# Performance work log

Hardware: AMD Instinct MI355X
Metric: run time of the kernel (lower is better)

The kernel has to match this reference:

```python
import jax, jax.numpy as jnp
import numpy as np

FONT_NUM = 190
HID = 256
HEADS = 2
EPS = 1e-5


def _bn(x, g, b, m, v):
    # eval-mode BatchNorm over the last (channel) axis
    return (x - m) * (g * jax.lax.rsqrt(v + EPS)) + b


def _gru(x, Wih, Whh, bih, bhh):
    # x: [B, S, D]; PyTorch gate order r, z, n. Returns all hidden states [B, S, H].
    B, S, _ = x.shape
    H = Whh.shape[1]
    xp = x @ Wih.T + bih  # [B, S, 3H] -- one big GEMM for all timesteps
    def step(h, xt):
        gh = h @ Whh.T + bhh
        xr, xz, xn = jnp.split(xt, 3, axis=-1)
        hr, hz, hn = jnp.split(gh, 3, axis=-1)
        r = jax.nn.sigmoid(xr + hr)
        z = jax.nn.sigmoid(xz + hz)
        n = jnp.tanh(xn + r * hn)
        h_new = (1.0 - z) * n + z * h
        return h_new, h_new
    h0 = jnp.zeros((B, H), x.dtype)
    _, hs = jax.lax.scan(step, h0, jnp.swapaxes(xp, 0, 1))
    return jnp.swapaxes(hs, 0, 1)


def _forward(img_emb, text_embs, len_mask, label_mask, labels,
             img_W, img_b, img_g, img_beta, img_m, img_v,
             g1_Wih, g1_Whh, g1_bih, g1_bhh, tl_W, tl_b,
             t_g, t_beta, t_m, t_v,
             g2_Wih, g2_Whh, g2_bih, g2_bhh, cl_W, cl_b,
             c_g, c_beta, c_m, c_v,
             attn_Win, attn_bin, attn_Wout, attn_bout, pred_W, pred_b):
    # img encoder: Linear -> BN -> (Dropout eval=id) -> ReLU
    img_fea = jax.nn.relu(_bn(img_emb @ img_W.T + img_b, img_g, img_beta, img_m, img_v))  # [B,H]
    # text encoder: GRU -> ReLU -> Linear, then BN+ReLU (torch does this in [B,C,S]; equivalent over channels)
    t = jax.nn.relu(_gru(text_embs, g1_Wih, g1_Whh, g1_bih, g1_bhh))
    t = t @ tl_W.T + tl_b
    text_fea = jax.nn.relu(_bn(t, t_g, t_beta, t_m, t_v))  # [B,S,H]
    len_info = len_mask.sum(axis=1)  # [B]
    # NOTE: sum over ALL timesteps divided by valid length (faithful to source)
    mean = text_fea.sum(axis=1) / len_info[:, None]  # [B,H]
    contrast = text_fea - mean[:, None, :]
    c = jax.nn.relu(_gru(contrast, g2_Wih, g2_Whh, g2_bih, g2_bhh))
    c = c @ cl_W.T + cl_b
    contrast_fea = jax.nn.relu(_bn(c, c_g, c_beta, c_m, c_v))  # [B,S,H]
    B, S, H = text_fea.shape
    hd = H // HEADS
    # batched 3-token self-attention: collapse the per-timestep python loop into one call
    tokens = jnp.stack([
        jnp.broadcast_to(img_fea[:, None, :], (B, S, H)), text_fea, contrast_fea
    ], axis=0).reshape(3, B * S, H)  # [3, N, H]
    Wq, Wk, Wv = jnp.split(attn_Win, 3, axis=0)
    bq, bk, bv = jnp.split(attn_bin, 3, axis=0)
    scale = 1.0 / jnp.sqrt(jnp.asarray(hd, tokens.dtype))
    q = (tokens @ Wq.T + bq).reshape(3, B * S, HEADS, hd) * scale
    k = (tokens @ Wk.T + bk).reshape(3, B * S, HEADS, hd)
    v = (tokens @ Wv.T + bv).reshape(3, B * S, HEADS, hd)
    scores = jnp.einsum('tnhd,snhd->nhts', q, k)  # [N, heads, 3, 3]
    attn = jax.nn.softmax(scores, axis=-1)
    o = jnp.einsum('nhts,snhd->tnhd', attn, v).reshape(3, B * S, H)
    o = o @ attn_Wout.T + attn_bout
    last = o.mean(axis=0).reshape(B, S, H)  # att_fea.mean(0) over the 3 tokens
    logits = last @ pred_W.T + pred_b  # [B,S,FONT_NUM]
    pred = jax.nn.softmax(logits, axis=-1)
    oh = jnp.maximum(label_mask, jax.nn.one_hot(labels, FONT_NUM, dtype=pred.dtype))
    loss = -(oh * jnp.log(pred)).sum(axis=-1)  # [B,S]
    loss = (loss * len_mask).sum(axis=1) / len_info
    return loss.mean()


def setup_inputs() -> dict:
    key = jax.random.key(0)
    ks = jax.random.split(key, 16)
    B, S, D, H = 128, 128, 2048, HID
    img_emb = jax.random.normal(ks[0], (B, D), jnp.float32)
    text_embs = jax.random.normal(ks[1], (B, S, D), jnp.float32)
    lengths = jax.random.randint(ks[2], (B,), S // 2, S + 1)
    len_mask = (jnp.arange(S)[None, :] < lengths[:, None]).astype(jnp.float32)
    labels = jax.random.randint(ks[3], (B, S), 0, FONT_NUM)
    label_mask = jnp.zeros((B, S, FONT_NUM), jnp.float32)
    w = lambda k, sh: jax.random.normal(k, sh, jnp.float32) * 0.02
    params = dict(
        img_W=w(ks[4], (H, D)), img_b=jnp.zeros((H,)),
        img_g=jnp.ones((H,)), img_beta=jnp.zeros((H,)), img_m=jnp.zeros((H,)), img_v=jnp.ones((H,)),
        g1_Wih=w(ks[5], (3 * (H // 2), D)), g1_Whh=w(ks[6], (3 * (H // 2), H // 2)),
        g1_bih=jnp.zeros((3 * (H // 2),)), g1_bhh=jnp.zeros((3 * (H // 2),)),
        tl_W=w(ks[7], (H, H // 2)), tl_b=jnp.zeros((H,)),
        t_g=jnp.ones((H,)), t_beta=jnp.zeros((H,)), t_m=jnp.zeros((H,)), t_v=jnp.ones((H,)),
        g2_Wih=w(ks[8], (3 * H, H)), g2_Whh=w(ks[9], (3 * H, H)),
        g2_bih=jnp.zeros((3 * H,)), g2_bhh=jnp.zeros((3 * H,)),
        cl_W=w(ks[10], (H, H)), cl_b=jnp.zeros((H,)),
        c_g=jnp.ones((H,)), c_beta=jnp.zeros((H,)), c_m=jnp.zeros((H,)), c_v=jnp.ones((H,)),
        attn_Win=w(ks[11], (3 * H, H)), attn_bin=jnp.zeros((3 * H,)),
        attn_Wout=w(ks[12], (H, H)), attn_bout=jnp.zeros((H,)),
        pred_W=w(ks[13], (FONT_NUM, H)), pred_b=jnp.zeros((FONT_NUM,)),
    )
    return dict(img_emb=img_emb, text_embs=text_embs, len_mask=len_mask,
                label_mask=label_mask, labels=labels, **params)


def reference(img_emb, text_embs, len_mask, label_mask, labels,
              img_W, img_b, img_g, img_beta, img_m, img_v,
              g1_Wih, g1_Whh, g1_bih, g1_bhh, tl_W, tl_b,
              t_g, t_beta, t_m, t_v,
              g2_Wih, g2_Whh, g2_bih, g2_bhh, cl_W, cl_b,
              c_g, c_beta, c_m, c_v,
              attn_Win, attn_bin, attn_Wout, attn_bout, pred_W, pred_b):
    return _forward(img_emb, text_embs, len_mask, label_mask, labels,
                    img_W, img_b, img_g, img_beta, img_m, img_v,
                    g1_Wih, g1_Whh, g1_bih, g1_bhh, tl_W, tl_b,
                    t_g, t_beta, t_m, t_v,
                    g2_Wih, g2_Whh, g2_bih, g2_bhh, cl_W, cl_b,
                    c_g, c_beta, c_m, c_v,
                    attn_Win, attn_bin, attn_Wout, attn_bout, pred_W, pred_b)
```

## Files before the change

### kernel.cpp

```cpp
#include <hip/hip_runtime.h>

typedef __attribute__((ext_vector_type(8))) short short8;
typedef __attribute__((ext_vector_type(4))) float f32x4;
typedef _Float16 f16;
typedef __attribute__((ext_vector_type(2))) _Float16 f16x2;
typedef __attribute__((ext_vector_type(8))) _Float16 f16x8;

__device__ inline float bf2f(unsigned short u){
  union{float f; unsigned u32;} x; x.u32 = ((unsigned)u) << 16; return x.f;
}
__device__ inline unsigned short f2bf(float f){
  union{float f; unsigned u;} x; x.f = f;
  unsigned r = (x.u + 0x7FFFu + ((x.u >> 16) & 1u)) >> 16;
  return (unsigned short)r;
}

#if defined(__has_builtin)
#  if __has_builtin(__builtin_amdgcn_fdot2)
#    define HAS_FDOT2 1
#  endif
#endif
__device__ inline float dot2f(f16x2 a, f16x2 b, float c){
#ifdef HAS_FDOT2
  return __builtin_amdgcn_fdot2(a, b, c, false);
#else
  return c + (float)a.x * (float)b.x + (float)a.y * (float)b.y;
#endif
}
__device__ inline f16x2 asf16x2(int v){ return __builtin_bit_cast(f16x2, v); }
__device__ inline int pack2(float lo, float hi){
  f16x2 p = f16x2{(f16)lo, (f16)hi};
  return __builtin_bit_cast(int, p);
}

__device__ inline float sigmoidf_(float x){ return 1.f / (1.f + __expf(-x)); }
__device__ inline float tanh_fast(float x){ float e = __expf(2.f * x); return 1.f - 2.f / (e + 1.f); }

__device__ inline float dpp_xor1(float x){
  return __int_as_float(__builtin_amdgcn_update_dpp(0, __float_as_int(x), 0xB1, 0xF, 0xF, true));
}
__device__ inline float dpp_xor2(float x){
  return __int_as_float(__builtin_amdgcn_update_dpp(0, __float_as_int(x), 0x4E, 0xF, 0xF, true));
}

__device__ inline void load8bf(const unsigned short* p, float* o){
  uint4 q = *(const uint4*)p;
  o[0]=bf2f((unsigned short)(q.x & 0xffffu)); o[1]=bf2f((unsigned short)(q.x >> 16));
  o[2]=bf2f((unsigned short)(q.y & 0xffffu)); o[3]=bf2f((unsigned short)(q.y >> 16));
  o[4]=bf2f((unsigned short)(q.z & 0xffffu)); o[5]=bf2f((unsigned short)(q.z >> 16));
  o[6]=bf2f((unsigned short)(q.w & 0xffffu)); o[7]=bf2f((unsigned short)(q.w >> 16));
}

#define GLL16(g, l) __builtin_amdgcn_global_load_lds(                      \
    (const __attribute__((address_space(1))) void*)(g),                    \
    (__attribute__((address_space(3))) void*)(l), 16, 0, 0)

__global__ __launch_bounds__(256) void conv_all_k(
    const float* __restrict__ s0, const float* __restrict__ s1,
    const float* __restrict__ s2, const float* __restrict__ s3,
    const float* __restrict__ s4, const float* __restrict__ s5,
    const float* __restrict__ s6, const float* __restrict__ s7,
    unsigned short* __restrict__ d0, unsigned short* __restrict__ d1,
    unsigned short* __restrict__ d2, f16* __restrict__ d3,
    unsigned short* __restrict__ d4, unsigned short* __restrict__ d5,
    unsigned short* __restrict__ d6, unsigned short* __restrict__ d7)
{
  int i = blockIdx.x * 256 + threadIdx.x;
  if (i >= 516096) return;
  const float* src; int local; int mode = 0; unsigned short* dst = nullptr; f16* dstf = nullptr;
  if (i < 196608)      { src = s0; local = i;           dst = d0; }
  else if (i < 204800) { src = s1; local = i - 196608;  dst = d1; }
  else if (i < 253952) { src = s2; local = i - 204800;  dst = d2; }
  else if (i < 303104) { src = s3; local = i - 253952;  dstf = d3; mode = 1; }
  else if (i < 319488) { src = s4; local = i - 303104;  dst = d4; }
  else if (i < 368640) { src = s5; local = i - 319488;  dst = d5; }
  else if (i < 385024) { src = s6; local = i - 368640;  dst = d6; }
  else                 { src = s7; local = i - 385024;  dst = d7; }
  float4 v = ((const float4*)src)[local];
  if (mode == 0) {
    union { unsigned short s[4]; uint2 q; } u;
    u.s[0]=f2bf(v.x); u.s[1]=f2bf(v.y); u.s[2]=f2bf(v.z); u.s[3]=f2bf(v.w);
    ((uint2*)dst)[local] = u.q;
  } else {
    union { f16 s[4]; uint2 q; } u;
    u.s[0]=(f16)v.x; u.s[1]=(f16)v.y; u.s[2]=(f16)v.z; u.s[3]=(f16)v.w;
    ((uint2*)dstf)[local] = u.q;
  }
}

__global__ __launch_bounds__(256) void pred_pad_k(const float* __restrict__ W,
                                                  const float* __restrict__ b,
                                                  unsigned short* __restrict__ Wd,
                                                  float* __restrict__ bd){
  int i = blockIdx.x * 256 + threadIdx.x;
  int j = i >> 8;
  Wd[i] = (j < 190) ? f2bf(W[i]) : (unsigned short)0;
  if (i < 192) bd[i] = (i < 190) ? b[i] : 0.f;
}

template<int OUT_T, bool BN, int A_MODE>
__global__ __launch_bounds__(256) void gemm128_k(
    const void* __restrict__ Ap, const unsigned short* __restrict__ Bw,
    const float* __restrict__ bias,
    const float* __restrict__ gam, const float* __restrict__ bet,
    const float* __restrict__ mu,  const float* __restrict__ var,
    void* __restrict__ Cp, int M, int N, int K)
{
  __shared__ __align__(16) unsigned short As[4096];
  __shared__ __align__(16) unsigned short Bs[4096];
  const int tid  = threadIdx.x;
  const int lane = tid & 63, wid = tid >> 6;
  const int wm = wid & 1, wn = wid >> 1;
  const int bm = blockIdx.y << 7, bn = blockIdx.x << 7;
  const int rA = tid >> 2, seg = tid & 3;

  f32x4 acc[4][4];
  #pragma unroll
  for (int i = 0; i < 4; i++)
    #pragma unroll
    for (int j = 0; j < 4; j++)
      acc[i][j] = f32x4{0.f, 0.f, 0.f, 0.f};

  const unsigned short* Abf = (const unsigned short*)Ap;
  const float* Af = (const float*)Ap;
  char* asb = (char*)As;
  char* bsb = (char*)Bs;
  char* asw = asb + wid * 1024;
  char* bsw = bsb + wid * 1024;

  for (int k0 = 0; k0 < K; k0 += 32) {
    if (A_MODE == 1) {
      #pragma unroll
      for (int beta = 0; beta < 2; beta++) {
        const float* src = Af + (size_t)(bm + rA + beta * 64) * K + k0 + seg * 8;
        float4 v0 = *(const float4*)src;
        float4 v1 = *(const float4*)(src + 4);
        union { unsigned short s[8]; uint4 q; } u;
        u.s[0]=f2bf(v0.x); u.s[1]=f2bf(v0.y); u.s[2]=f2bf(v0.z); u.s[3]=f2bf(v0.w);
        u.s[4]=f2bf(v1.x); u.s[5]=f2bf(v1.y); u.s[6]=f2bf(v1.z); u.s[7]=f2bf(v1.w);
        *(uint4*)(asb + beta * 4096 + tid * 16) = u.q;
      }
    } else if (A_MODE == 2) {
      const float* mrow = mu + (size_t)(bm >> 7) * 256 + k0 + seg * 8;
      float4 m0 = *(const float4*)mrow;
      float4 m1 = *(const float4*)(mrow + 4);
      #pragma unroll
      for (int beta = 0; beta < 2; beta++) {
        const unsigned short* src = Abf + (size_t)(bm + rA + beta * 64) * K + k0 + seg * 8;
        float av[8];
        load8bf(src, av);
        union { unsigned short s[8]; uint4 q; } u;
        u.s[0]=f2bf(av[0]-m0.x); u.s[1]=f2bf(av[1]-m0.y); u.s[2]=f2bf(av[2]-m0.z); u.s[3]=f2bf(av[3]-m0.w);
        u.s[4]=f2bf(av[4]-m1.x); u.s[5]=f2bf(av[5]-m1.y); u.s[6]=f2bf(av[6]-m1.z); u.s[7]=f2bf(av[7]-m1.w);
        *(uint4*)(asb + beta * 4096 + tid * 16) = u.q;
      }
    } else {
      GLL16(Abf + (size_t)(bm + rA)      * K + k0 + seg * 8, asw);
      GLL16(Abf + (size_t)(bm + rA + 64) * K + k0 + seg * 8, asw + 4096);
    }
    GLL16(Bw + (size_t)(bn + rA)      * K + k0 + seg * 8, bsw);
    GLL16(Bw + (size_t)(bn + rA + 64) * K + k0 + seg * 8, bsw + 4096);
    __syncthreads();

    short8 a[4], b[4];
    #pragma unroll
    for (int f = 0; f < 4; f++) {
      int ra = wm * 64 + f * 16 + (lane & 15);
      a[f] = *(const short8*)(asb + ra * 64 + (lane >> 4) * 16);
      int rb = wn * 64 + f * 16 + (lane & 15);
      b[f] = *(const short8*)(bsb + rb * 64 + (lane >> 4) * 16);
    }
    #pragma unroll
    for (int fm = 0; fm < 4; fm++)
      #pragma unroll
      for (int fn = 0; fn < 4; fn++)
        acc[fm][fn] = __builtin_amdgcn_mfma_f32_16x16x32_bf16(a[fm], b[fn], acc[fm][fn], 0, 0, 0);
    __syncthreads();
  }

  #pragma unroll
  for (int fn = 0; fn < 4; fn++) {
    int col = bn + wn * 64 + fn * 16 + (lane & 15);
    float bs = bias[col];
    float sc = 1.f, sh = 0.f;
    if (BN) { float s = gam[col] * rsqrtf(var[col] + 1e-5f); sc = s; sh = bet[col] - mu[col] * s; }
    #pragma unroll
    for (int fm = 0; fm < 4; fm++) {
      int row = bm + wm * 64 + fm * 16 + ((lane >> 4) << 2);
      #pragma unroll
      for (int j = 0; j < 4; j++) {
        float v = acc[fm][fn][j] + bs;
        if (BN) { v = v * sc + sh; v = fmaxf(v, 0.f); }
        size_t idx = (size_t)(row + j) * N + col;
        if (OUT_T == 1) ((f16*)Cp)[idx] = (f16)v;
        else            ((unsigned short*)Cp)[idx] = f2bf(v);
      }
    }
  }
}

template<int OUT_T, bool BN, bool AF32>
__global__ __launch_bounds__(256) void gemm_k(
    const void* __restrict__ Ap, const unsigned short* __restrict__ Bw,
    const float* __restrict__ bias,
    const float* __restrict__ gam, const float* __restrict__ bet,
    const float* __restrict__ mu,  const float* __restrict__ var,
    void* __restrict__ Cp, int M, int N, int K)
{
  __shared__ unsigned short As[64][40];
  __shared__ unsigned short Bs[64][40];
  const int tid  = threadIdx.x;
  const int lane = tid & 63, wid = tid >> 6;
  const int wm = wid & 1, wn = wid >> 1;
  const int bm = blockIdx.y << 6, bn = blockIdx.x << 6;
  const int srow = tid >> 2, sseg = tid & 3;

  f32x4 acc[2][2];
  #pragma unroll
  for (int i = 0; i < 2; i++)
    #pragma unroll
    for (int j = 0; j < 2; j++)
      acc[i][j] = f32x4{0.f, 0.f, 0.f, 0.f};

  const unsigned short* Abf = (const unsigned short*)Ap;
  const float* Af = (const float*)Ap;

  for (int k0 = 0; k0 < K; k0 += 32) {
    if (AF32) {
      const float* src = Af + (size_t)(bm + srow) * K + k0 + sseg * 8;
      float4 v0 = *(const float4*)(src);
      float4 v1 = *(const float4*)(src + 4);
      union { unsigned short s[8]; uint4 q; } u;
      u.s[0]=f2bf(v0.x); u.s[1]=f2bf(v0.y); u.s[2]=f2bf(v0.z); u.s[3]=f2bf(v0.w);
      u.s[4]=f2bf(v1.x); u.s[5]=f2bf(v1.y); u.s[6]=f2bf(v1.z); u.s[7]=f2bf(v1.w);
      *(uint4*)&As[srow][sseg * 8] = u.q;
    } else {
      *(uint4*)&As[srow][sseg * 8] =
          *(const uint4*)(Abf + (size_t)(bm + srow) * K + k0 + sseg * 8);
    }
    *(uint4*)&Bs[srow][sseg * 8] =
        *(const uint4*)(Bw + (size_t)(bn + srow) * K + k0 + sseg * 8);
    __syncthreads();

    short8 a0 = *(const short8*)&As[wm * 32 +      (lane & 15)][(lane >> 4) * 8];
    short8 a1 = *(const short8*)&As[wm * 32 + 16 + (lane & 15)][(lane >> 4) * 8];
    short8 b0 = *(const short8*)&Bs[wn * 32 +      (lane & 15)][(lane >> 4) * 8];
    short8 b1 = *(const short8*)&Bs[wn * 32 + 16 + (lane & 15)][(lane >> 4) * 8];
    acc[0][0] = __builtin_amdgcn_mfma_f32_16x16x32_bf16(a0, b0, acc[0][0], 0, 0, 0);
    acc[0][1] = __builtin_amdgcn_mfma_f32_16x16x32_bf16(a0, b1, acc[0][1], 0, 0, 0);
    acc[1][0] = __builtin_amdgcn_mfma_f32_16x16x32_bf16(a1, b0, acc[1][0], 0, 0, 0);
    acc[1][1] = __builtin_amdgcn_mfma_f32_16x16x32_bf16(a1, b1, acc[1][1], 0, 0, 0);
    __syncthreads();
  }

  #pragma unroll
  for (int fn = 0; fn < 2; fn++) {
    int col = bn + wn * 32 + fn * 16 + (lane & 15);
    float bs = bias[col];
    float sc = 1.f, sh = 0.f;
    if (BN) { float s = gam[col] * rsqrtf(var[col] + 1e-5f); sc = s; sh = bet[col] - mu[col] * s; }
    #pragma unroll
    for (int fm = 0; fm < 2; fm++) {
      int row = bm + wm * 32 + fm * 16 + ((lane >> 4) << 2);
      #pragma unroll
      for (int j = 0; j < 4; j++) {
        float v = acc[fm][fn][j] + bs;
        if (BN) { v = v * sc + sh; v = fmaxf(v, 0.f); }
        size_t idx = (size_t)(row + j) * N + col;
        if (OUT_T == 0)      ((float*)Cp)[idx] = v;
        else if (OUT_T == 1) ((f16*)Cp)[idx]   = (f16)v;
        else                 ((unsigned short*)Cp)[idx] = f2bf(v);
      }
    }
  }
}

__global__ __launch_bounds__(512, 2) void gru2_scan_k(
    const f16* __restrict__ Wf,
    const float* __restrict__ bhh,
    const f16* __restrict__ xp, unsigned short* __restrict__ hs_relu)
{
  const int b = blockIdx.x;
  const int tid = threadIdx.x;
  const int jj = tid >> 1, kh = tid & 1;
  __shared__ __align__(16) f16 hbuf[2][256];
  __shared__ __align__(16) char wnl[16 * 512 * 16];

  {
    const f16* src = Wf + (size_t)(512 + jj) * 256 + kh * 128;
    #pragma unroll
    for (int c = 0; c < 16; c++)
      *(uint4*)(wnl + c * 8192 + tid * 16) = *(const uint4*)(src + c * 8);
  }

  int wri[64], wzi[64];
  #pragma unroll
  for (int i = 0; i < 16; i++) {
    const int kb = kh * 128 + i * 8;
    uint4 q;
    q = *(const uint4*)&Wf[(size_t)(jj      ) * 256 + kb];
    wri[4*i+0] = (int)q.x; wri[4*i+1] = (int)q.y; wri[4*i+2] = (int)q.z; wri[4*i+3] = (int)q.w;
    q = *(const uint4*)&Wf[(size_t)(jj + 256) * 256 + kb];
    wzi[4*i+0] = (int)q.x; wzi[4*i+1] = (int)q.y; wzi[4*i+2] = (int)q.z; wzi[4*i+3] = (int)q.w;
  }
  #pragma unroll
  for (int i = 0; i < 64; i++)
    asm volatile("" : "+v"(wri[i]), "+v"(wzi[i]));

  const float br = bhh[jj], bz = bhh[jj + 256], bn2 = bhh[jj + 512];
  if (tid < 256) hbuf[0][tid] = (f16)0.f;
  float hprev = 0.f;
  f16 pxr = (f16)0.f, pxz = (f16)0.f, pxn = (f16)0.f;
  if (kh == 0) {
    const f16* x0 = xp + (size_t)(b * 128) * 768;
    pxr = x0[jj]; pxz = x0[256 + jj]; pxn = x0[512 + jj];
  }
  __syncthreads();
  int cur = 0;
  const char* mybase = wnl + tid * 16;
  for (int t = 0; t < 128; t++) {
    float xr = (float)pxr, xz = (float)pxz, xn = (float)pxn;
    if (kh == 0) {
      const int tn = (t < 127) ? (t + 1) : 127;
      const f16* xnr = xp + (size_t)(b * 128 + tn) * 768;
      pxr = xnr[jj]; pxz = xnr[256 + jj]; pxn = xnr[512 + jj];
    }
    const char* hb = (const char*)hbuf[cur] + kh * 256;
    float ar = 0.f, az = 0.f, an = 0.f;
    #pragma unroll
    for (int i = 0; i < 16; i++) {
      f16x8 hv = *(const f16x8*)(hb + i * 16);
      f16x8 wv = *(const f16x8*)(mybase + i * 8192);
      #pragma unroll
      for (int u = 0; u < 4; u++) {
        f16x2 hp = f16x2{hv[2*u], hv[2*u+1]};
        ar = dot2f(asf16x2(wri[4*i+u]), hp, ar);
        az = dot2f(asf16x2(wzi[4*i+u]), hp, az);
        an = dot2f(f16x2{wv[2*u], wv[2*u+1]}, hp, an);
      }
    }
    ar += dpp_xor1(ar);
    az += dpp_xor1(az);
    an += dpp_xor1(an);
    if (kh == 0) {
      float r = sigmoidf_(xr + ar + br);
      float z = sigmoidf_(xz + az + bz);
      float n = tanh_fast(xn + r * (an + bn2));
      float hnew = (1.f - z) * n + z * hprev;
      hprev = hnew;
      hbuf[cur ^ 1][jj] = (f16)hnew;
      hs_relu[(size_t)(b * 128 + t) * 256 + jj] = f2bf(fmaxf(hnew, 0.f));
    }
    __syncthreads();
    cur ^= 1;
  }
}

__global__ __launch_bounds__(512, 4) void gru1_scan_k(
    const float* __restrict__ Whh, const float* __restrict__ bhh,
    const f16* __restrict__ xp, unsigned short* __restrict__ hs_relu)
{
  const int b = blockIdx.x;
  const int tid = threadIdx.x;
  const int jj = tid >> 2, kh = tid & 3;
  __shared__ __align__(16) f16 hbuf[2][128];

  int wri[16], wzi[16], wni[16];
  #pragma unroll
  for (int i = 0; i < 4; i++) {
    const int kb = kh * 32 + i * 8;
    float4 f0, f1;
    f0 = *(const float4*)&Whh[(size_t)(jj      ) * 128 + kb];
    f1 = *(const float4*)&Whh[(size_t)(jj      ) * 128 + kb + 4];
    wri[4*i+0] = pack2(f0.x, f0.y); wri[4*i+1] = pack2(f0.z, f0.w);
    wri[4*i+2] = pack2(f1.x, f1.y); wri[4*i+3] = pack2(f1.z, f1.w);
    f0 = *(const float4*)&Whh[(size_t)(jj + 128) * 128 + kb];
    f1 = *(const float4*)&Whh[(size_t)(jj + 128) * 128 + kb + 4];
    wzi[4*i+0] = pack2(f0.x, f0.y); wzi[4*i+1] = pack2(f0.z, f0.w);
    wzi[4*i+2] = pack2(f1.x, f1.y); wzi[4*i+3] = pack2(f1.z, f1.w);
    f0 = *(const float4*)&Whh[(size_t)(jj + 256) * 128 + kb];
    f1 = *(const float4*)&Whh[(size_t)(jj + 256) * 128 + kb + 4];
    wni[4*i+0] = pack2(f0.x, f0.y); wni[4*i+1] = pack2(f0.z, f0.w);
    wni[4*i+2] = pack2(f1.x, f1.y); wni[4*i+3] = pack2(f1.z, f1.w);
  }
  #pragma unroll
  for (int i = 0; i < 16; i++)
    asm volatile("" : "+v"(wri[i]), "+v"(wzi[i]), "+v"(wni[i]));

  const float br = bhh[jj], bz = bhh[jj + 128], bn2 = bhh[jj + 256];
  if (tid < 128) hbuf[0][tid] = (f16)0.f;
  float hprev = 0.f;
  f16 pxr = (f16)0.f, pxz = (f16)0.f, pxn = (f16)0.f;
  if (kh == 0) {
    const f16* x0 = xp + (size_t)(b * 128) * 384;
    pxr = x0[jj]; pxz = x0[128 + jj]; pxn = x0[256 + jj];
  }
  __syncthreads();
  int cur = 0;
  for (int t = 0; t < 128; t++) {
    float xr = (float)pxr, xz = (float)pxz, xn = (float)pxn;
    if (kh == 0) {
      const int tn = (t < 127) ? (t + 1) : 127;
      const f16* xnr = xp + (size_t)(b * 128 + tn) * 384;
      pxr = xnr[jj]; pxz = xnr[128 + jj]; pxn = xnr[256 + jj];
    }
    const char* hb = (const char*)hbuf[cur] + kh * 64;
    float ar = 0.f, az = 0.f, an = 0.f;
    #pragma unroll
    for (int c = 0; c < 4; c++) {
      f16x8 hv = *(const f16x8*)(hb + c * 16);
      #pragma unroll
      for (int u = 0; u < 4; u++) {
        f16x2 hp = f16x2{hv[2*u], hv[2*u+1]};
        ar = dot2f(asf16x2(wri[4*c+u]), hp, ar);
        az = dot2f(asf16x2(wzi[4*c+u]), hp, az);
        an = dot2f(asf16x2(wni[4*c+u]), hp, an);
      }
    }
    ar += dpp_xor1(ar); ar += dpp_xor2(ar);
    az += dpp_xor1(az); az += dpp_xor2(az);
    an += dpp_xor1(an); an += dpp_xor2(an);
    if (kh == 0) {
      float r = sigmoidf_(xr + ar + br);
      float z = sigmoidf_(xz + az + bz);
      float n = tanh_fast(xn + r * (an + bn2));
      float hnew = (1.f - z) * n + z * hprev;
      hprev = hnew;
      hbuf[cur ^ 1][jj] = (f16)hnew;
      hs_relu[(size_t)(b * 128 + t) * 128 + jj] = f2bf(fmaxf(hnew, 0.f));
    }
    __syncthreads();
    cur ^= 1;
  }
}

__global__ __launch_bounds__(256) void mean_k(const unsigned short* __restrict__ tf,
                                              const float* __restrict__ len_mask,
                                              float* __restrict__ mean,
                                              float* __restrict__ len_info){
  int b = blockIdx.x, c = threadIdx.x;
  float acc = 0.f;
  for (int s = 0; s < 128; s++) acc += bf2f(tf[(size_t)(b * 128 + s) * 256 + c]);
  float len = 0.f;
  for (int s = 0; s < 128; s++) len += len_mask[b * 128 + s];
  mean[b * 256 + c] = acc / len;
  if (c == 0) len_info[b] = len;
}

__global__ __launch_bounds__(256) void attn_k(const unsigned short* __restrict__ qkv0,
                                              const unsigned short* __restrict__ qkv1,
                                              const unsigned short* __restrict__ qkv2,
                                              unsigned short* __restrict__ osum){
  int i = blockIdx.x * 256 + threadIdx.x;
  int h = i & 1; int n = i >> 1; int b = n >> 7;
  const unsigned short* t0 = qkv0 + (size_t)b * 768 + h * 128;
  const unsigned short* t1 = qkv1 + (size_t)n * 768 + h * 128;
  const unsigned short* t2 = qkv2 + (size_t)n * 768 + h * 128;
  float sc[3][3];
  #pragma unroll
  for (int a = 0; a < 3; a++)
    #pragma unroll
    for (int s = 0; s < 3; s++) sc[a][s] = 0.f;
  #pragma unroll 1
  for (int dc = 0; dc < 16; dc++) {
    float q[3][8], k[3][8];
    load8bf(t0 + dc * 8, q[0]); load8bf(t1 + dc * 8, q[1]); load8bf(t2 + dc * 8, q[2]);
    load8bf(t0 + 256 + dc * 8, k[0]); load8bf(t1 + 256 + dc * 8, k[1]); load8bf(t2 + 256 + dc * 8, k[2]);
    #pragma unroll
    for (int a = 0; a < 3; a++)
      #pragma unroll
      for (int s = 0; s < 3; s++) {
        float d = 0.f;
        #pragma unroll
        for (int e = 0; e < 8; e++) d += q[a][e] * k[s][e];
        sc[a][s] += d;
      }
  }
  const float scale = 0.08838834764831845f;
  float w[3] = {0.f, 0.f, 0.f};
  #pragma unroll
  for (int a = 0; a < 3; a++) {
    float s0 = sc[a][0] * scale, s1 = sc[a][1] * scale, s2 = sc[a][2] * scale;
    float m = fmaxf(s0, fmaxf(s1, s2));
    float e0 = __expf(s0 - m), e1 = __expf(s1 - m), e2 = __expf(s2 - m);
    float inv = 1.f / (e0 + e1 + e2);
    w[0] += e0 * inv; w[1] += e1 * inv; w[2] += e2 * inv;
  }
  w[0] *= (1.f / 3.f); w[1] *= (1.f / 3.f); w[2] *= (1.f / 3.f);
  unsigned short* op = osum + (size_t)n * 256 + h * 128;
  #pragma unroll 1
  for (int dc = 0; dc < 16; dc++) {
    float v0[8], v1[8], v2[8];
    load8bf(t0 + 512 + dc * 8, v0); load8bf(t1 + 512 + dc * 8, v1); load8bf(t2 + 512 + dc * 8, v2);
    union { unsigned short s[8]; uint4 q; } u;
    #pragma unroll
    for (int e = 0; e < 8; e++) u.s[e] = f2bf(w[0] * v0[e] + w[1] * v1[e] + w[2] * v2[e]);
    *(uint4*)(op + dc * 8) = u.q;
  }
}

__global__ __launch_bounds__(64) void loss_k(const float* __restrict__ logits,
                                             const float* __restrict__ label_mask,
                                             const int* __restrict__ labels,
                                             float* __restrict__ loss_raw){
  int r = blockIdx.x; int j = threadIdx.x;
  int lab = labels[r];
  float l[3]; float m = -1e30f;
  #pragma unroll
  for (int q = 0; q < 3; q++) {
    int c = j + q * 64;
    float lv = (c < 190) ? logits[(size_t)r * 192 + c] : -1e30f;
    l[q] = lv; m = fmaxf(m, lv);
  }
  #pragma unroll
  for (int off = 32; off; off >>= 1) m = fmaxf(m, __shfl_xor(m, off));
  float se = 0.f, soh = 0.f, dot = 0.f;
  #pragma unroll
  for (int q = 0; q < 3; q++) {
    int c = j + q * 64;
    if (c < 190) {
      se += expf(l[q] - m);
      float oh = fmaxf(label_mask[(size_t)r * 190 + c], (c == lab) ? 1.f : 0.f);
      soh += oh; dot += oh * l[q];
    }
  }
  #pragma unroll
  for (int off = 32; off; off >>= 1) {
    se += __shfl_xor(se, off); soh += __shfl_xor(soh, off); dot += __shfl_xor(dot, off);
  }
  if (j == 0) loss_raw[r] = (m + logf(se)) * soh - dot;
}

__global__ __launch_bounds__(256) void final_k(const float* __restrict__ loss_raw,
                                               const float* __restrict__ len_mask,
                                               const float* __restrict__ len_info,
                                               float* __restrict__ out){
  __shared__ float sh[256];
  int t = threadIdx.x;
  float acc = 0.f;
  for (int i = t; i < 16384; i += 256) acc += loss_raw[i] * len_mask[i] / len_info[i >> 7];
  sh[t] = acc; __syncthreads();
  for (int s = 128; s; s >>= 1) { if (t < s) sh[t] += sh[t + s]; __syncthreads(); }
  if (t == 0) out[0] = sh[0] / 128.f;
}

extern "C" void kernel_launch(void* const* d_in, const int* in_sizes, int n_in,
                              void* d_out, int out_size, void* d_ws, size_t ws_size,
                              hipStream_t stream)
{
  const float* img_emb    = (const float*)d_in[0];
  const float* text_embs  = (const float*)d_in[1];
  const float* len_mask   = (const float*)d_in[2];
  const float* label_mask = (const float*)d_in[3];
  const int*   labels     = (const int*)  d_in[4];
  const float* img_W   = (const float*)d_in[5];
  const float* img_b   = (const float*)d_in[6];
  const float* img_g   = (const float*)d_in[7];
  const float* img_be  = (const float*)d_in[8];
  const float* img_m   = (const float*)d_in[9];
  const float* img_v   = (const float*)d_in[10];
  const float* g1_Wih  = (const float*)d_in[11];
  const float* g1_Whh  = (const float*)d_in[12];
  const float* g1_bih  = (const float*)d_in[13];
  const float* g1_bhh  = (const float*)d_in[14];
  const float* tl_W    = (const float*)d_in[15];
  const float* tl_b    = (const float*)d_in[16];
  const float* t_g     = (const float*)d_in[17];
  const float* t_be    = (const float*)d_in[18];
  const float* t_m     = (const float*)d_in[19];
  const float* t_v     = (const float*)d_in[20];
  const float* g2_Wih  = (const float*)d_in[21];
  const float* g2_Whh  = (const float*)d_in[22];
  const float* g2_bih  = (const float*)d_in[23];
  const float* g2_bhh  = (const float*)d_in[24];
  const float* cl_W    = (const float*)d_in[25];
  const float* cl_b    = (const float*)d_in[26];
  const float* c_g     = (const float*)d_in[27];
  const float* c_be    = (const float*)d_in[28];
  const float* c_m     = (const float*)d_in[29];
  const float* c_v     = (const float*)d_in[30];
  const float* a_Win   = (const float*)d_in[31];
  const float* a_bin   = (const float*)d_in[32];
  const float* a_Wout  = (const float*)d_in[33];
  const float* a_bout  = (const float*)d_in[34];
  const float* pred_W  = (const float*)d_in[35];
  const float* pred_b  = (const float*)d_in[36];

  char* ws = (char*)d_ws;
  size_t o = 0;
  auto alloc = [&](size_t sz){ size_t r = o; o += (sz + 255) & ~(size_t)255; return r; };

  size_t o_g1Wih = alloc(384ull*2048*2);
  size_t o_tlW   = alloc(256ull*128*2);
  size_t o_g2Wih = alloc(768ull*256*2);
  size_t o_g2Whh = alloc(768ull*256*2);
  size_t o_clW   = alloc(256ull*256*2);
  size_t o_aWin  = alloc(768ull*256*2);
  size_t o_aWout = alloc(256ull*256*2);
  size_t o_imgW  = alloc(256ull*2048*2);
  size_t o_predW = alloc(192ull*256*2);
  size_t o_predb = alloc(192ull*4);
  size_t o_imgfea= alloc(128ull*256*2);
  size_t o_mean  = alloc(128ull*256*4);
  size_t o_len   = alloc(128ull*4);
  size_t o_R0    = alloc(33554432ull);
  size_t o_RB    = alloc(25165824ull);
  size_t o_tfea  = alloc(16384ull*256*2);
  size_t o_qkv1  = alloc(16384ull*768*2);
  size_t o_cfea  = alloc(16384ull*256*2);
  size_t o_qkv0  = alloc(128ull*768*2);
  size_t o_loss  = alloc(16384ull*4);
  (void)ws_size; (void)in_sizes; (void)n_in; (void)out_size;

  unsigned short* g1Wih_bf = (unsigned short*)(ws + o_g1Wih);
  unsigned short* tlW_bf   = (unsigned short*)(ws + o_tlW);
  unsigned short* g2Wih_bf = (unsigned short*)(ws + o_g2Wih);
  f16*            g2Whh_f  = (f16*)(ws + o_g2Whh);
  unsigned short* clW_bf   = (unsigned short*)(ws + o_clW);
  unsigned short* aWin_bf  = (unsigned short*)(ws + o_aWin);
  unsigned short* aWout_bf = (unsigned short*)(ws + o_aWout);
  unsigned short* imgW_bf  = (unsigned short*)(ws + o_imgW);
  unsigned short* predW_bf = (unsigned short*)(ws + o_predW);
  float*          predb_p  = (float*)(ws + o_predb);
  unsigned short* img_fea  = (unsigned short*)(ws + o_imgfea);
  float*          meanb    = (float*)(ws + o_mean);
  float*          len_info = (float*)(ws + o_len);
  f16*            xp2      = (f16*)(ws + o_R0);
  unsigned short* hs2      = (unsigned short*)(ws + o_R0 + 25165824ull);
  unsigned short* osum     = (unsigned short*)(ws + o_R0);
  unsigned short* lastb    = (unsigned short*)(ws + o_R0 + 8388608ull);
  f16*            xp1      = (f16*)(ws + o_RB);
  unsigned short* hs1      = (unsigned short*)(ws + o_RB + 12582912ull);
  unsigned short* qkv2     = (unsigned short*)(ws + o_RB);
  unsigned short* tfea     = (unsigned short*)(ws + o_tfea);
  unsigned short* qkv1     = (unsigned short*)(ws + o_qkv1);
  float*          logits   = (float*)(ws + o_qkv1);
  unsigned short* cfea     = (unsigned short*)(ws + o_cfea);
  unsigned short* qkv0     = (unsigned short*)(ws + o_qkv0);
  float*          loss_raw = (float*)(ws + o_loss);
  float*          outp     = (float*)d_out;

  conv_all_k<<<2016, 256, 0, stream>>>(
      g1_Wih, tl_W, g2_Wih, g2_Whh, cl_W, a_Win, a_Wout, img_W,
      g1Wih_bf, tlW_bf, g2Wih_bf, g2Whh_f, clW_bf, aWin_bf, aWout_bf, imgW_bf);
  pred_pad_k<<<192, 256, 0, stream>>>(pred_W, pred_b, predW_bf, predb_p);

  gemm128_k<2, true, 1><<<dim3(2, 1), 256, 0, stream>>>(
      img_emb, imgW_bf, img_b, img_g, img_be, img_m, img_v, img_fea, 128, 256, 2048);

  gemm128_k<1, false, 1><<<dim3(3, 128), 256, 0, stream>>>(
      text_embs, g1Wih_bf, g1_bih, nullptr, nullptr, nullptr, nullptr, xp1, 16384, 384, 2048);

  gru1_scan_k<<<128, 512, 0, stream>>>(g1_Whh, g1_bhh, xp1, hs1);

  gemm128_k<2, true, 0><<<dim3(2, 128), 256, 0, stream>>>(
      hs1, tlW_bf, tl_b, t_g, t_be, t_m, t_v, tfea, 16384, 256, 128);

  mean_k<<<128, 256, 0, stream>>>(tfea, len_mask, meanb, len_info);

  gemm128_k<1, false, 2><<<dim3(6, 128), 256, 0, stream>>>(
      tfea, g2Wih_bf, g2_bih, nullptr, nullptr, meanb, nullptr, xp2, 16384, 768, 256);

  gru2_scan_k<<<128, 512, 0, stream>>>(g2Whh_f, g2_bhh, xp2, hs2);

  gemm128_k<2, true, 0><<<dim3(2, 128), 256, 0, stream>>>(
      hs2, clW_bf, cl_b, c_g, c_be, c_m, c_v, cfea, 16384, 256, 256);

  gemm128_k<2, false, 0><<<dim3(6, 1), 256, 0, stream>>>(
      img_fea, aWin_bf, a_bin, nullptr, nullptr, nullptr, nullptr, qkv0, 128, 768, 256);
  gemm128_k<2, false, 0><<<dim3(6, 128), 256, 0, stream>>>(
      tfea, aWin_bf, a_bin, nullptr, nullptr, nullptr, nullptr, qkv1, 16384, 768, 256);
  gemm128_k<2, false, 0><<<dim3(6, 128), 256, 0, stream>>>(
      cfea, aWin_bf, a_bin, nullptr, nullptr, nullptr, nullptr, qkv2, 16384, 768, 256);

  attn_k<<<128, 256, 0, stream>>>(qkv0, qkv1, qkv2, osum);

  gemm128_k<2, false, 0><<<dim3(2, 128), 256, 0, stream>>>(
      osum, aWout_bf, a_bout, nullptr, nullptr, nullptr, nullptr, lastb, 16384, 256, 256);

  gemm_k<0, false, false><<<dim3(3, 256), 256, 0, stream>>>(
      lastb, predW_bf, predb_p, nullptr, nullptr, nullptr, nullptr, logits, 16384, 192, 256);

  loss_k<<<16384, 64, 0, stream>>>(logits, label_mask, labels, loss_raw);
  final_k<<<1, 256, 0, stream>>>(loss_raw, len_mask, len_info, outp);
}
```

Before: 619.9 us.

## Stream GRU2 z/n weights from global and widen GRU1 to 1024 threads

In the second GRU scan, only the r-gate weights stay in registers. The z and n gate weights are no longer held in registers or in a 128KB LDS copy. They are streamed from global (L1/L2) on every timestep through a small software-prefetched register ring, which drops the large shared allocation and cuts register pressure. The first GRU scan now splits each hidden unit's dot product across 8 lanes instead of 4, using 1024 threads and an extra ds_swizzle reduction step to shorten the per-step serial dot product. The cost is repeated global weight reads on every recurrent step in GRU2, and an extra cross-lane reduction plus heavier block-wide barriers in GRU1.

```diff
diff --git a/kernel.cpp b/kernel.cpp
--- a/kernel.cpp
+++ b/kernel.cpp
@@ -41,6 +41,9 @@
 }
 __device__ inline float dpp_xor2(float x){
   return __int_as_float(__builtin_amdgcn_update_dpp(0, __float_as_int(x), 0x4E, 0xF, 0xF, true));
+}
+__device__ inline float swz_xor4(float x){
+  return __int_as_float(__builtin_amdgcn_ds_swizzle(__float_as_int(x), 0x101F));
 }
 
 __device__ inline void load8bf(const unsigned short* p, float* o){
@@ -284,28 +287,19 @@
   const int tid = threadIdx.x;
   const int jj = tid >> 1, kh = tid & 1;
   __shared__ __align__(16) f16 hbuf[2][256];
-  __shared__ __align__(16) char wnl[16 * 512 * 16];
-
-  {
-    const f16* src = Wf + (size_t)(512 + jj) * 256 + kh * 128;
-    #pragma unroll
-    for (int c = 0; c < 16; c++)
-      *(uint4*)(wnl + c * 8192 + tid * 16) = *(const uint4*)(src + c * 8);
-  }
-
-  int wri[64], wzi[64];
+
+  int wri[64];
   #pragma unroll
   for (int i = 0; i < 16; i++) {
-    const int kb = kh * 128 + i * 8;
-    uint4 q;
-    q = *(const uint4*)&Wf[(size_t)(jj      ) * 256 + kb];
+    uint4 q = *(const uint4*)&Wf[(size_t)jj * 256 + kh * 128 + i * 8];
     wri[4*i+0] = (int)q.x; wri[4*i+1] = (int)q.y; wri[4*i+2] = (int)q.z; wri[4*i+3] = (int)q.w;
-    q = *(const uint4*)&Wf[(size_t)(jj + 256) * 256 + kb];
-    wzi[4*i+0] = (int)q.x; wzi[4*i+1] = (int)q.y; wzi[4*i+2] = (int)q.z; wzi[4*i+3] = (int)q.w;
   }
   #pragma unroll
   for (int i = 0; i < 64; i++)
-    asm volatile("" : "+v"(wri[i]), "+v"(wzi[i]));
+    asm volatile("" : "+v"(wri[i]));
+
+  const f16* zsrc = Wf + (size_t)(256 + jj) * 256 + kh * 128;
+  const f16* nsrc = Wf + (size_t)(512 + jj) * 256 + kh * 128;
 
   const float br = bhh[jj], bz = bhh[jj + 256], bn2 = bhh[jj + 512];
   if (tid < 256) hbuf[0][tid] = (f16)0.f;
@@ -317,7 +311,6 @@
   }
   __syncthreads();
   int cur = 0;
-  const char* mybase = wnl + tid * 16;
   for (int t = 0; t < 128; t++) {
     float xr = (float)pxr, xz = (float)pxz, xn = (float)pxn;
     if (kh == 0) {
@@ -325,18 +318,29 @@
       const f16* xnr = xp + (size_t)(b * 128 + tn) * 768;
       pxr = xnr[jj]; pxz = xnr[256 + jj]; pxn = xnr[512 + jj];
     }
+    uint4 zb[4], nb[4];
+    #pragma unroll
+    for (int c = 0; c < 4; c++) {
+      zb[c] = *(const uint4*)(zsrc + c * 8);
+      nb[c] = *(const uint4*)(nsrc + c * 8);
+    }
     const char* hb = (const char*)hbuf[cur] + kh * 256;
     float ar = 0.f, az = 0.f, an = 0.f;
     #pragma unroll
     for (int i = 0; i < 16; i++) {
       f16x8 hv = *(const f16x8*)(hb + i * 16);
-      f16x8 wv = *(const f16x8*)(mybase + i * 8192);
+      f16x8 zv = __builtin_bit_cast(f16x8, zb[i & 3]);
+      f16x8 nv = __builtin_bit_cast(f16x8, nb[i & 3]);
+      if (i < 12) {
+        zb[i & 3] = *(const uint4*)(zsrc + (i + 4) * 8);
+        nb[i & 3] = *(const uint4*)(nsrc + (i + 4) * 8);
+      }
       #pragma unroll
       for (int u = 0; u < 4; u++) {
         f16x2 hp = f16x2{hv[2*u], hv[2*u+1]};
         ar = dot2f(asf16x2(wri[4*i+u]), hp, ar);
-        az = dot2f(asf16x2(wzi[4*i+u]), hp, az);
-        an = dot2f(f16x2{wv[2*u], wv[2*u+1]}, hp, an);
+        az = dot2f(f16x2{zv[2*u], zv[2*u+1]}, hp, az);
+        an = dot2f(f16x2{nv[2*u], nv[2*u+1]}, hp, an);
       }
     }
     ar += dpp_xor1(ar);
@@ -356,19 +360,19 @@
   }
 }
 
-__global__ __launch_bounds__(512, 4) void gru1_scan_k(
+__global__ __launch_bounds__(1024) void gru1_scan_k(
     const float* __restrict__ Whh, const float* __restrict__ bhh,
     const f16* __restrict__ xp, unsigned short* __restrict__ hs_relu)
 {
   const int b = blockIdx.x;
   const int tid = threadIdx.x;
-  const int jj = tid >> 2, kh = tid & 3;
+  const int jj = tid >> 3, kh = tid & 7;
   __shared__ __align__(16) f16 hbuf[2][128];
 
-  int wri[16], wzi[16], wni[16];
-  #pragma unroll
-  for (int i = 0; i < 4; i++) {
-    const int kb = kh * 32 + i * 8;
+  int wri[8], wzi[8], wni[8];
+  #pragma unroll
+  for (int i = 0; i < 2; i++) {
+    const int kb = kh * 16 + i * 8;
     float4 f0, f1;
     f0 = *(const float4*)&Whh[(size_t)(jj      ) * 128 + kb];
     f1 = *(const float4*)&Whh[(size_t)(jj      ) * 128 + kb + 4];
@@ -384,7 +388,7 @@
     wni[4*i+2] = pack2(f1.x, f1.y); wni[4*i+3] = pack2(f1.z, f1.w);
   }
   #pragma unroll
-  for (int i = 0; i < 16; i++)
+  for (int i = 0; i < 8; i++)
     asm volatile("" : "+v"(wri[i]), "+v"(wzi[i]), "+v"(wni[i]));
 
   const float br = bhh[jj], bz = bhh[jj + 128], bn2 = bhh[jj + 256];
@@ -404,10 +408,10 @@
       const f16* xnr = xp + (size_t)(b * 128 + tn) * 384;
       pxr = xnr[jj]; pxz = xnr[128 + jj]; pxn = xnr[256 + jj];
     }
-    const char* hb = (const char*)hbuf[cur] + kh * 64;
+    const char* hb = (const char*)hbuf[cur] + kh * 32;
     float ar = 0.f, az = 0.f, an = 0.f;
     #pragma unroll
-    for (int c = 0; c < 4; c++) {
+    for (int c = 0; c < 2; c++) {
       f16x8 hv = *(const f16x8*)(hb + c * 16);
       #pragma unroll
       for (int u = 0; u < 4; u++) {
@@ -417,9 +421,9 @@
         an = dot2f(asf16x2(wni[4*c+u]), hp, an);
       }
     }
-    ar += dpp_xor1(ar); ar += dpp_xor2(ar);
-    az += dpp_xor1(az); az += dpp_xor2(az);
-    an += dpp_xor1(an); an += dpp_xor2(an);
+    ar += dpp_xor1(ar); ar += dpp_xor2(ar); ar += swz_xor4(ar);
+    az += dpp_xor1(az); az += dpp_xor2(az); az += swz_xor4(az);
+    an += dpp_xor1(an); an += dpp_xor2(an); an += swz_xor4(an);
     if (kh == 0) {
       float r = sigmoidf_(xr + ar + br);
       float z = sigmoidf_(xz + az + bz);
@@ -651,7 +655,7 @@
   gemm128_k<1, false, 1><<<dim3(3, 128), 256, 0, stream>>>(
       text_embs, g1Wih_bf, g1_bih, nullptr, nullptr, nullptr, nullptr, xp1, 16384, 384, 2048);
 
-  gru1_scan_k<<<128, 512, 0, stream>>>(g1_Whh, g1_bhh, xp1, hs1);
+  gru1_scan_k<<<128, 1024, 0, stream>>>(g1_Whh, g1_bhh, xp1, hs1);
 
   gemm128_k<2, true, 0><<<dim3(2, 128), 256, 0, stream>>>(
       hs1, tlW_bf, tl_b, t_g, t_be, t_m, t_v, tfea, 16384, 256, 128);
```

Result: slower. 645.5 us (+4.1%).

## Merge three QKV projection GEMMs into one launch; stream GRU2 n-gate weights from global

Applied to the files above, without the earlier changes.

Replaces the three separate QKV projection GEMM launches (image, text and contrast features) with a single kernel whose grid rows select the input and output, which saves two launches and fills the GPU better. In the second GRU scan, the n-gate weights are no longer staged in 128KB of shared memory. Each timestep instead loads them from global memory (cache-resident) through a small rolling register prefetch. This cuts LDS use so more blocks can be resident, but it adds global loads on the serial recurrence path.

```diff
diff --git a/kernel.cpp b/kernel.cpp
--- a/kernel.cpp
+++ b/kernel.cpp
@@ -199,6 +199,78 @@
   }
 }
 
+__global__ __launch_bounds__(256) void gemmqkv_k(
+    const unsigned short* __restrict__ tfea, const unsigned short* __restrict__ cfea,
+    const unsigned short* __restrict__ imgf, const unsigned short* __restrict__ Bw,
+    const float* __restrict__ bias,
+    unsigned short* __restrict__ q1, unsigned short* __restrict__ q2,
+    unsigned short* __restrict__ q0)
+{
+  const int N = 768, K = 256;
+  __shared__ __align__(16) unsigned short As[4096];
+  __shared__ __align__(16) unsigned short Bs[4096];
+  const int tid  = threadIdx.x;
+  const int lane = tid & 63, wid = tid >> 6;
+  const int wm = wid & 1, wn = wid >> 1;
+  const int y = blockIdx.y;
+  const unsigned short* Abf; unsigned short* Cp; int bm;
+  if (y < 128)      { Abf = tfea; Cp = q1; bm = y << 7; }
+  else if (y < 256) { Abf = cfea; Cp = q2; bm = (y - 128) << 7; }
+  else              { Abf = imgf; Cp = q0; bm = 0; }
+  const int bn = blockIdx.x << 7;
+  const int rA = tid >> 2, seg = tid & 3;
+
+  f32x4 acc[4][4];
+  #pragma unroll
+  for (int i = 0; i < 4; i++)
+    #pragma unroll
+    for (int j = 0; j < 4; j++)
+      acc[i][j] = f32x4{0.f, 0.f, 0.f, 0.f};
+
+  char* asb = (char*)As;
+  char* bsb = (char*)Bs;
+  char* asw = asb + wid * 1024;
+  char* bsw = bsb + wid * 1024;
+
+  for (int k0 = 0; k0 < K; k0 += 32) {
+    GLL16(Abf + (size_t)(bm + rA)      * K + k0 + seg * 8, asw);
+    GLL16(Abf + (size_t)(bm + rA + 64) * K + k0 + seg * 8, asw + 4096);
+    GLL16(Bw + (size_t)(bn + rA)      * K + k0 + seg * 8, bsw);
+    GLL16(Bw + (size_t)(bn + rA + 64) * K + k0 + seg * 8, bsw + 4096);
+    __syncthreads();
+
+    short8 a[4], b[4];
+    #pragma unroll
+    for (int f = 0; f < 4; f++) {
+      int ra = wm * 64 + f * 16 + (lane & 15);
+      a[f] = *(const short8*)(asb + ra * 64 + (lane >> 4) * 16);
+      int rb = wn * 64 + f * 16 + (lane & 15);
+      b[f] = *(const short8*)(bsb + rb * 64 + (lane >> 4) * 16);
+    }
+    #pragma unroll
+    for (int fm = 0; fm < 4; fm++)
+      #pragma unroll
+      for (int fn = 0; fn < 4; fn++)
+        acc[fm][fn] = __builtin_amdgcn_mfma_f32_16x16x32_bf16(a[fm], b[fn], acc[fm][fn], 0, 0, 0);
+    __syncthreads();
+  }
+
+  #pragma unroll
+  for (int fn = 0; fn < 4; fn++) {
+    int col = bn + wn * 64 + fn * 16 + (lane & 15);
+    float bs = bias[col];
+    #pragma unroll
+    for (int fm = 0; fm < 4; fm++) {
+      int row = bm + wm * 64 + fm * 16 + ((lane >> 4) << 2);
+      #pragma unroll
+      for (int j = 0; j < 4; j++) {
+        float v = acc[fm][fn][j] + bs;
+        Cp[(size_t)(row + j) * N + col] = f2bf(v);
+      }
+    }
+  }
+}
+
 template<int OUT_T, bool BN, bool AF32>
 __global__ __launch_bounds__(256) void gemm_k(
     const void* __restrict__ Ap, const unsigned short* __restrict__ Bw,
@@ -284,14 +356,6 @@
   const int tid = threadIdx.x;
   const int jj = tid >> 1, kh = tid & 1;
   __shared__ __align__(16) f16 hbuf[2][256];
-  __shared__ __align__(16) char wnl[16 * 512 * 16];
-
-  {
-    const f16* src = Wf + (size_t)(512 + jj) * 256 + kh * 128;
-    #pragma unroll
-    for (int c = 0; c < 16; c++)
-      *(uint4*)(wnl + c * 8192 + tid * 16) = *(const uint4*)(src + c * 8);
-  }
 
   int wri[64], wzi[64];
   #pragma unroll
@@ -307,6 +371,8 @@
   for (int i = 0; i < 64; i++)
     asm volatile("" : "+v"(wri[i]), "+v"(wzi[i]));
 
+  const f16* nsrc = Wf + (size_t)(512 + jj) * 256 + kh * 128;
+
   const float br = bhh[jj], bz = bhh[jj + 256], bn2 = bhh[jj + 512];
   if (tid < 256) hbuf[0][tid] = (f16)0.f;
   float hprev = 0.f;
@@ -317,7 +383,6 @@
   }
   __syncthreads();
   int cur = 0;
-  const char* mybase = wnl + tid * 16;
   for (int t = 0; t < 128; t++) {
     float xr = (float)pxr, xz = (float)pxz, xn = (float)pxn;
     if (kh == 0) {
@@ -325,18 +390,23 @@
       const f16* xnr = xp + (size_t)(b * 128 + tn) * 768;
       pxr = xnr[jj]; pxz = xnr[256 + jj]; pxn = xnr[512 + jj];
     }
+    uint4 nb[4];
+    #pragma unroll
+    for (int c = 0; c < 4; c++) nb[c] = *(const uint4*)(nsrc + c * 8);
+
     const char* hb = (const char*)hbuf[cur] + kh * 256;
     float ar = 0.f, az = 0.f, an = 0.f;
     #pragma unroll
     for (int i = 0; i < 16; i++) {
       f16x8 hv = *(const f16x8*)(hb + i * 16);
-      f16x8 wv = *(const f16x8*)(mybase + i * 8192);
+      f16x8 nv = __builtin_bit_cast(f16x8, nb[i & 3]);
+      if (i < 12) nb[i & 3] = *(const uint4*)(nsrc + (i + 4) * 8);
       #pragma unroll
       for (int u = 0; u < 4; u++) {
         f16x2 hp = f16x2{hv[2*u], hv[2*u+1]};
         ar = dot2f(asf16x2(wri[4*i+u]), hp, ar);
         az = dot2f(asf16x2(wzi[4*i+u]), hp, az);
-        an = dot2f(f16x2{wv[2*u], wv[2*u+1]}, hp, an);
+        an = dot2f(f16x2{nv[2*u], nv[2*u+1]}, hp, an);
       }
     }
     ar += dpp_xor1(ar);
@@ -666,12 +736,8 @@
   gemm128_k<2, true, 0><<<dim3(2, 128), 256, 0, stream>>>(
       hs2, clW_bf, cl_b, c_g, c_be, c_m, c_v, cfea, 16384, 256, 256);
 
-  gemm128_k<2, false, 0><<<dim3(6, 1), 256, 0, stream>>>(
-      img_fea, aWin_bf, a_bin, nullptr, nullptr, nullptr, nullptr, qkv0, 128, 768, 256);
-  gemm128_k<2, false, 0><<<dim3(6, 128), 256, 0, stream>>>(
-      tfea, aWin_bf, a_bin, nullptr, nullptr, nullptr, nullptr, qkv1, 16384, 768, 256);
-  gemm128_k<2, false, 0><<<dim3(6, 128), 256, 0, stream>>>(
-      cfea, aWin_bf, a_bin, nullptr, nullptr, nullptr, nullptr, qkv2, 16384, 768, 256);
+  gemmqkv_k<<<dim3(6, 257), 256, 0, stream>>>(
+      tfea, cfea, img_fea, aWin_bf, a_bin, qkv1, qkv2, qkv0);
 
   attn_k<<<128, 256, 0, stream>>>(qkv0, qkv1, qkv2, osum);
 
```

Result: faster. 596.1 us (-3.8%).
